# Optimization experiments

Measured on AMD Instinct MI355X. Metric: run time of the kernel, lower is better.

## Reference

```python
import jax, jax.numpy as jnp
import numpy as np

B, N, DIM, H, DH, M = 2, 2048, 1024, 16, 64, 512
INNER = H * DH  # 1024
KV = M + 1 + N  # xl mem + null kv + sequence = 2561


def rotate_half(x):
    x1, x2 = jnp.split(x, 2, axis=-1)
    return jnp.concatenate([-x2, x1], axis=-1)


def apply_rotary_pos_emb(pos, t):
    return t * jnp.cos(pos) + rotate_half(t) * jnp.sin(pos)


def setup_inputs() -> dict:
    key = jax.random.key(0)
    ks = jax.random.split(key, 8)
    return {
        "x": jax.random.normal(ks[0], (B, N, DIM), jnp.float32),
        "rotary_q": jax.random.uniform(ks[1], (N, DH), jnp.float32) * 6.28,
        "rotary_k": jax.random.uniform(ks[2], (KV, DH), jnp.float32) * 6.28,
        "xl_memories": jax.random.normal(ks[3], (2, B, H, M, DH), jnp.float32) * 0.02,
        "Wq": jax.random.normal(ks[4], (DIM, INNER), jnp.float32) * 0.02,
        "Wkv": jax.random.normal(ks[5], (DIM, 2 * INNER), jnp.float32) * 0.02,
        "Wout": jax.random.normal(ks[6], (INNER, INNER), jnp.float32) * 0.02,
        "null_kv": jax.random.normal(ks[7], (2, H, DH), jnp.float32),
    }


def reference(x, rotary_q, rotary_k, xl_memories, Wq, Wkv, Wout, null_kv):
    # QKV projections (no bias, matching keras Dense(use_bias=False))
    q = (x @ Wq).reshape(B, N, H, DH).transpose(0, 2, 1, 3)  # b h n d
    k, v = jnp.split(x @ Wkv, 2, axis=-1)
    k = k.reshape(B, N, H, DH).transpose(0, 2, 1, 3)
    v = v.reshape(B, N, H, DH).transpose(0, 2, 1, 3)

    # prepend learned null key/value (1 token)
    nk = jnp.broadcast_to(null_kv[0][None, :, None, :], (B, H, 1, DH))
    nv = jnp.broadcast_to(null_kv[1][None, :, None, :], (B, H, 1, DH))
    k = jnp.concatenate([nk, k], axis=2)
    v = jnp.concatenate([nv, v], axis=2)

    next_xl_memories = jnp.stack([k, v])  # [2, b, h, 1+n, d]

    # prepend XL memories along key axis
    k = jnp.concatenate([xl_memories[0], k], axis=2)  # b h kv d
    v = jnp.concatenate([xl_memories[1], v], axis=2)

    # inline rotary embedding on q and (full) k
    q = apply_rotary_pos_emb(rotary_q, q)
    k = apply_rotary_pos_emb(rotary_k, k)

    # causal attention with bottom-right aligned mask (mem/null tokens visible)
    scale = DH ** -0.5
    sim = jnp.einsum('bhid,bhjd->bhij', q, k) * scale  # b h n kv
    i = jnp.arange(N)[:, None]
    j = jnp.arange(KV)[None, :]
    causal_ok = j <= (i + (KV - N))
    sim = jnp.where(causal_ok, sim, jnp.finfo(sim.dtype).min)
    attn = jax.nn.softmax(sim, axis=-1)
    out = jnp.einsum('bhij,bhjd->bhid', attn, v)  # b h n d

    out = out.transpose(0, 2, 1, 3).reshape(B, N, INNER)
    return out @ Wout, next_xl_memories
```

## Files before the change

kernel.cpp:

```cpp
#include <hip/hip_runtime.h>
#include <hip/hip_bf16.h>


typedef short v8s __attribute__((ext_vector_type(8)));
typedef float v4f __attribute__((ext_vector_type(4)));

__device__ __forceinline__ float bf2f(unsigned short x) {
  return __uint_as_float(((unsigned)x) << 16);
}
__device__ __forceinline__ unsigned short f2bf(float f) {
  unsigned u = __float_as_uint(f);
  u += 0x7FFFu + ((u >> 16) & 1u);
  return (unsigned short)(u >> 16);
}

#if __has_builtin(__builtin_amdgcn_exp2f)
#define EXP2(x) __builtin_amdgcn_exp2f(x)
#else
#define EXP2(x) exp2f(x)
#endif

__device__ __forceinline__ void gld_lds16(const void* g, void* l) {
  __builtin_amdgcn_global_load_lds(
      (const __attribute__((address_space(1))) unsigned int*)g,
      (__attribute__((address_space(3))) unsigned int*)l, 16, 0, 0);
}

__device__ __forceinline__ unsigned pk_bf16(float lo, float hi) {
  union { __hip_bfloat162 h; unsigned u; } cv;
  cv.h = __float22bfloat162_rn(make_float2(lo, hi));
  return cv.u;
}

__global__ __launch_bounds__(256) void cvt_bf16(
    const float* __restrict__ S, unsigned short* __restrict__ D, int n4)
{
  const int i = blockIdx.x * 256 + threadIdx.x;
  if (i < n4) {
    const float4 v = ((const float4*)S)[i];
    ushort4 o;
    o.x = f2bf(v.x); o.y = f2bf(v.y); o.z = f2bf(v.z); o.w = f2bf(v.w);
    ((ushort4*)D)[i] = o;
  }
}

template <typename CT>
__global__ __launch_bounds__(256, 2) void gemm_bf16(
    const unsigned short* __restrict__ A,
    const unsigned short* __restrict__ WT,
    CT* __restrict__ C,
    int K, int ldc)
{
  __shared__ unsigned short As[128 * 64];
  __shared__ unsigned short Bs[128 * 64];
  const int tid  = threadIdx.x;
  const int wave = tid >> 6, lane = tid & 63;
  const int l15  = lane & 15, quad = lane >> 4;
  const int wm   = wave >> 1, wn = wave & 1;
  const int row0 = blockIdx.x * 128, col0 = blockIdx.y * 128;
  const int lrow = lane >> 3;
  const int gsw  = (lane & 7) ^ lrow;

  v4f acc[4][4];
  const v4f vzero = {0.f, 0.f, 0.f, 0.f};
#pragma unroll
  for (int i = 0; i < 4; ++i)
#pragma unroll
    for (int j = 0; j < 4; ++j) acc[i][j] = vzero;

  for (int k0 = 0; k0 < K; k0 += 64) {
    __syncthreads();
#pragma unroll
    for (int ro = 0; ro < 4; ++ro) {
      const int chunk = wave * 4 + ro;
      const int arow  = chunk * 8 + lrow;
      gld_lds16(A  + (size_t)(row0 + arow) * K + k0 + gsw * 8, As + chunk * 512);
      gld_lds16(WT + (size_t)(col0 + arow) * K + k0 + gsw * 8, Bs + chunk * 512);
    }
    __syncthreads();

    v8s af[4][2], bf[4][2];
#pragma unroll
    for (int tm = 0; tm < 4; ++tm) {
      const int r = wm * 64 + tm * 16 + l15;
#pragma unroll
      for (int kk = 0; kk < 2; ++kk) {
        const int slot = (kk * 4 + quad) ^ (r & 7);
        af[tm][kk] = *(const v8s*)(As + r * 64 + slot * 8);
      }
    }
#pragma unroll
    for (int tn = 0; tn < 4; ++tn) {
      const int r = wn * 64 + tn * 16 + l15;
#pragma unroll
      for (int kk = 0; kk < 2; ++kk) {
        const int slot = (kk * 4 + quad) ^ (r & 7);
        bf[tn][kk] = *(const v8s*)(Bs + r * 64 + slot * 8);
      }
    }
#pragma unroll
    for (int kk = 0; kk < 2; ++kk)
#pragma unroll
      for (int tm = 0; tm < 4; ++tm)
#pragma unroll
        for (int tn = 0; tn < 4; ++tn)
          acc[tm][tn] = __builtin_amdgcn_mfma_f32_16x16x32_bf16(
              af[tm][kk], bf[tn][kk], acc[tm][tn], 0, 0, 0);
  }

#pragma unroll
  for (int tm = 0; tm < 4; ++tm)
#pragma unroll
    for (int tn = 0; tn < 4; ++tn)
#pragma unroll
      for (int r = 0; r < 4; ++r) {
        const int row = row0 + wm * 64 + tm * 16 + quad * 4 + r;
        const int col = col0 + wn * 64 + tn * 16 + l15;
        if constexpr (sizeof(CT) == 2)
          C[(size_t)row * ldc + col] = (CT)f2bf(acc[tm][tn][r]);
        else
          C[(size_t)row * ldc + col] = (CT)acc[tm][tn][r];
      }
}

__global__ __launch_bounds__(256) void transpose_wt(
    const float* __restrict__ S0,
    const float* __restrict__ S1,
    int c0, int c1, int K,
    unsigned short* __restrict__ D)
{
  __shared__ float T[64][65];
  const int k0 = blockIdx.x * 64, n0 = blockIdx.y * 64;
  const int tid = threadIdx.x;
#pragma unroll
  for (int ro = 0; ro < 4; ++ro) {
    const int idx = ro * 256 + tid;
    const int kr = idx >> 4, ch = idx & 15;
    const int n = n0 + ch * 4;
    float4 val;
    if (n < c0) val = *(const float4*)(S0 + (size_t)(k0 + kr) * c0 + n);
    else        val = *(const float4*)(S1 + (size_t)(k0 + kr) * c1 + (n - c0));
    T[kr][ch * 4 + 0] = val.x; T[kr][ch * 4 + 1] = val.y;
    T[kr][ch * 4 + 2] = val.z; T[kr][ch * 4 + 3] = val.w;
  }
  __syncthreads();
#pragma unroll
  for (int ro = 0; ro < 2; ++ro) {
    const int idx = ro * 256 + tid;
    const int nl = idx >> 3, ch = idx & 7;
    __align__(16) unsigned short tmp[8];
#pragma unroll
    for (int e = 0; e < 8; ++e) tmp[e] = f2bf(T[ch * 8 + e][nl]);
    *(uint4*)(D + (size_t)(n0 + nl) * K + k0 + ch * 8) = *(const uint4*)tmp;
  }
}

__global__ __launch_bounds__(256) void assemble(
    const unsigned short* __restrict__ QKV,
    const float* __restrict__ rq,
    const float* __restrict__ rk,
    const float* __restrict__ xlm,
    const float* __restrict__ nkv,
    unsigned short* __restrict__ Qrot,
    unsigned short* __restrict__ Kf,
    unsigned short* __restrict__ Vn,
    float* __restrict__ nxl)
{
  const int gw = blockIdx.x * 4 + (threadIdx.x >> 6);
  const int d  = threadIdx.x & 63;
  const int RK = 32 * 2561;
  const int RQ = 32 * 2048;
  if (gw < RK) {
    const int bh = gw / 2561;
    const int j  = gw - bh * 2561;
    const int b  = bh >> 4, h = bh & 15;
    float kx, vx;
    if (j < 512) {
      const size_t i0 = (((size_t)(b * 16 + h)) * 512 + j) * 64 + d;
      kx = xlm[i0];
      vx = xlm[1048576 + i0];
    } else if (j == 512) {
      kx = nkv[h * 64 + d];
      vx = nkv[1024 + h * 64 + d];
    } else {
      const size_t rowb = ((size_t)(b * 2048 + (j - 513))) * 3072;
      kx = bf2f(QKV[rowb + 1024 + h * 64 + d]);
      vx = bf2f(QKV[rowb + 2048 + h * 64 + d]);
    }
    Vn[(((size_t)bh) * 2561 + j) * 64 + d] = f2bf(vx);
    if (j >= 512) {
      const size_t o0 = (((size_t)(b * 16 + h)) * 2049 + (j - 512)) * 64 + d;
      nxl[o0] = kx;
      nxl[4196352 + o0] = vx;
    }
    const float ang = rk[j * 64 + d];
    const float cs = __cosf(ang), sn = __sinf(ang);
    const float part = __shfl_xor(kx, 32);
    const float kr = kx * cs + (d < 32 ? -part : part) * sn;
    Kf[(((size_t)bh) * 2624 + j) * 64 + d] = f2bf(kr);
  } else if (gw < RK + RQ) {
    const int g2 = gw - RK;
    const int bh = g2 >> 11, n = g2 & 2047;
    const int b  = bh >> 4, h = bh & 15;
    const float qx = bf2f(QKV[((size_t)(b * 2048 + n)) * 3072 + h * 64 + d]);
    const float ang = rq[n * 64 + d];
    const float cs = __cosf(ang), sn = __sinf(ang);
    const float part = __shfl_xor(qx, 32);
    const float qr = qx * cs + (d < 32 ? -part : part) * sn;
    Qrot[(((size_t)bh) * 2048 + n) * 64 + d] = f2bf(qr * 0.18033688f);
  } else {
    const int g3 = gw - RK - RQ;
    const int bh = g3 / 63;
    const int jj = 2561 + (g3 - bh * 63);
    Kf[(((size_t)bh) * 2624 + jj) * 64 + d] = 0;
  }
}

__global__ __launch_bounds__(256) void transpose_v(
    const unsigned short* __restrict__ Vn,
    unsigned short* __restrict__ VTp)
{
  __shared__ unsigned short T[64][72];
  const int j0 = blockIdx.x * 64;
  const int bh = blockIdx.y;
  const int tid = threadIdx.x;
#pragma unroll
  for (int ro = 0; ro < 2; ++ro) {
    const int idx = ro * 256 + tid;
    const int jr = idx >> 3, ch = idx & 7;
    uint4 val = make_uint4(0, 0, 0, 0);
    if (j0 + jr < 2561)
      val = *(const uint4*)(Vn + (((size_t)bh) * 2561 + j0 + jr) * 64 + ch * 8);
    *(uint4*)(&T[jr][ch * 8]) = val;
  }
  __syncthreads();
#pragma unroll
  for (int ro = 0; ro < 2; ++ro) {
    const int idx = ro * 256 + tid;
    const int dl = idx >> 3, ch = idx & 7;
    __align__(16) unsigned short tmp[8];
#pragma unroll
    for (int e = 0; e < 8; ++e) {
      const int kappa = ch * 8 + e;
      const int sig = (kappa & 32) + ((e & 4) << 2) + ((ch & 3) << 2) + (e & 3);
      tmp[e] = T[sig][dl];
    }
    *(uint4*)(VTp + (((size_t)bh) * 64 + dl) * 2624 + j0 + ch * 8) = *(const uint4*)tmp;
  }
}

__global__ __launch_bounds__(256, 4) void attn_fa(
    const unsigned short* __restrict__ Qr,
    const unsigned short* __restrict__ Kf,
    const unsigned short* __restrict__ VTp,
    unsigned short* __restrict__ Ao)
{
  const int bh = blockIdx.y;
  const int qb = 31 - (int)((blockIdx.x + blockIdx.y) & 31);
  const int b = bh >> 4, h = bh & 15;
  __shared__ unsigned short Ks[2][2][32 * 72];
  __shared__ unsigned short Vs[2][2][64 * 40];
  const int tid = threadIdx.x;
  const int wave = tid >> 6;
  const int wr  = wave & 1;
  const int kvh = wave >> 1;
  const int lane = tid & 63;
  const int l15 = lane & 15, quad = lane >> 4;
  const v4f vzero = {0.f, 0.f, 0.f, 0.f};

  v8s qf00, qf01, qf10, qf11;
  {
    const unsigned short* Qg0 =
        Qr + (((size_t)bh) * 2048 + qb * 64 + wr * 32 + l15) * 64;
    qf00 = *(const v8s*)(Qg0 + quad * 8);
    qf01 = *(const v8s*)(Qg0 + 32 + quad * 8);
    const unsigned short* Qg1 = Qg0 + 16 * 64;
    qf10 = *(const v8s*)(Qg1 + quad * 8);
    qf11 = *(const v8s*)(Qg1 + 32 + quad * 8);
  }
  const int qb0 = qb * 64 + wr * 32 + l15 + 513;

  v4f O00 = vzero, O01 = vzero, O02 = vzero, O03 = vzero;
  v4f O10 = vzero, O11 = vzero, O12 = vzero, O13 = vzero;
  v4f Ol0 = vzero, Ol1 = vzero;
  const short one_bf = (short)0x3F80;
  const v8s ones = {one_bf, one_bf, one_bf, one_bf,
                    one_bf, one_bf, one_bf, one_bf};

  const unsigned short* Kg0 = Kf + (size_t)bh * 2624 * 64;
  const unsigned short* Vg0 = VTp + (size_t)bh * 64 * 2624;
  const int nt32  = (2 * qb + 19 <= 81) ? (2 * qb + 19) : 81;
  const int nh    = (nt32 + 1) >> 1;
  const int tbase = kvh ? nh : 0;
  const int tcnt  = kvh ? (nt32 - nh) : nh;
  const int tfast = 2 * qb + wr + 15;

  const int ptid = tid & 127;
  const int krow = ptid >> 3, ksch = ptid & 7;
  const int vrow = ptid >> 2, vscv = ptid & 3;
  uint4 kk0, kk1, vv0, vv1;

#define PREFETCH(t)                                                          \
  {                                                                          \
    const int j0p = (t) * 32;                                                \
    kk0 = *(const uint4*)(Kg0 + (size_t)(j0p + krow)      * 64 + ksch * 8);  \
    kk1 = *(const uint4*)(Kg0 + (size_t)(j0p + krow + 16) * 64 + ksch * 8);  \
    vv0 = *(const uint4*)(Vg0 + (size_t)(vrow)      * 2624 + j0p + vscv * 8);\
    vv1 = *(const uint4*)(Vg0 + (size_t)(vrow + 32) * 2624 + j0p + vscv * 8);\
  }
#define STAGE(bi)                                                            \
  {                                                                          \
    *(uint4*)(Ks[kvh][bi] + (krow)      * 72 + ksch * 8) = kk0;              \
    *(uint4*)(Ks[kvh][bi] + (krow + 16) * 72 + ksch * 8) = kk1;              \
    *(uint4*)(Vs[kvh][bi] + (vrow)      * 40 + vscv * 8) = vv0;              \
    *(uint4*)(Vs[kvh][bi] + (vrow + 32) * 40 + vscv * 8) = vv1;              \
  }

  auto compute_tile = [&](const unsigned short* Ksb, const unsigned short* Vsb,
                          int t) {
    v4f s00, s01, s10, s11;
    {
      const v8s ka0 = *(const v8s*)(Ksb + l15 * 72 + quad * 8);
      const v8s ka1 = *(const v8s*)(Ksb + l15 * 72 + 32 + quad * 8);
      v4f c = vzero;
      c = __builtin_amdgcn_mfma_f32_16x16x32_bf16(ka0, qf00, c, 0, 0, 0);
      c = __builtin_amdgcn_mfma_f32_16x16x32_bf16(ka1, qf01, c, 0, 0, 0);
      s00 = c;
      c = vzero;
      c = __builtin_amdgcn_mfma_f32_16x16x32_bf16(ka0, qf10, c, 0, 0, 0);
      c = __builtin_amdgcn_mfma_f32_16x16x32_bf16(ka1, qf11, c, 0, 0, 0);
      s10 = c;
      const v8s kb0 = *(const v8s*)(Ksb + (16 + l15) * 72 + quad * 8);
      const v8s kb1 = *(const v8s*)(Ksb + (16 + l15) * 72 + 32 + quad * 8);
      c = vzero;
      c = __builtin_amdgcn_mfma_f32_16x16x32_bf16(kb0, qf00, c, 0, 0, 0);
      c = __builtin_amdgcn_mfma_f32_16x16x32_bf16(kb1, qf01, c, 0, 0, 0);
      s01 = c;
      c = vzero;
      c = __builtin_amdgcn_mfma_f32_16x16x32_bf16(kb0, qf10, c, 0, 0, 0);
      c = __builtin_amdgcn_mfma_f32_16x16x32_bf16(kb1, qf11, c, 0, 0, 0);
      s11 = c;
    }

    if (t > tfast) {
      const int j0 = t * 32 + quad * 4;
#pragma unroll
      for (int r = 0; r < 4; ++r) {
        s00[r] = (j0 + r      <= qb0)      ? s00[r] : -1e30f;
        s01[r] = (j0 + 16 + r <= qb0)      ? s01[r] : -1e30f;
        s10[r] = (j0 + r      <= qb0 + 16) ? s10[r] : -1e30f;
        s11[r] = (j0 + 16 + r <= qb0 + 16) ? s11[r] : -1e30f;
      }
    }

    union PK { unsigned u[4]; v8s s8; };
    PK p0, p1;
    p0.u[0] = pk_bf16(EXP2(s00[0]), EXP2(s00[1]));
    p0.u[1] = pk_bf16(EXP2(s00[2]), EXP2(s00[3]));
    p0.u[2] = pk_bf16(EXP2(s01[0]), EXP2(s01[1]));
    p0.u[3] = pk_bf16(EXP2(s01[2]), EXP2(s01[3]));
    p1.u[0] = pk_bf16(EXP2(s10[0]), EXP2(s10[1]));
    p1.u[1] = pk_bf16(EXP2(s10[2]), EXP2(s10[3]));
    p1.u[2] = pk_bf16(EXP2(s11[0]), EXP2(s11[1]));
    p1.u[3] = pk_bf16(EXP2(s11[2]), EXP2(s11[3]));

    {
      const v8s vf0 = *(const v8s*)(Vsb + l15 * 40 + quad * 8);
      O00 = __builtin_amdgcn_mfma_f32_16x16x32_bf16(p0.s8, vf0, O00, 0, 0, 0);
      O10 = __builtin_amdgcn_mfma_f32_16x16x32_bf16(p1.s8, vf0, O10, 0, 0, 0);
      const v8s vf1 = *(const v8s*)(Vsb + (16 + l15) * 40 + quad * 8);
      O01 = __builtin_amdgcn_mfma_f32_16x16x32_bf16(p0.s8, vf1, O01, 0, 0, 0);
      O11 = __builtin_amdgcn_mfma_f32_16x16x32_bf16(p1.s8, vf1, O11, 0, 0, 0);
      const v8s vf2 = *(const v8s*)(Vsb + (32 + l15) * 40 + quad * 8);
      O02 = __builtin_amdgcn_mfma_f32_16x16x32_bf16(p0.s8, vf2, O02, 0, 0, 0);
      O12 = __builtin_amdgcn_mfma_f32_16x16x32_bf16(p1.s8, vf2, O12, 0, 0, 0);
      const v8s vf3 = *(const v8s*)(Vsb + (48 + l15) * 40 + quad * 8);
      O03 = __builtin_amdgcn_mfma_f32_16x16x32_bf16(p0.s8, vf3, O03, 0, 0, 0);
      O13 = __builtin_amdgcn_mfma_f32_16x16x32_bf16(p1.s8, vf3, O13, 0, 0, 0);
    }
    Ol0 = __builtin_amdgcn_mfma_f32_16x16x32_bf16(p0.s8, ones, Ol0, 0, 0, 0);
    Ol1 = __builtin_amdgcn_mfma_f32_16x16x32_bf16(p1.s8, ones, Ol1, 0, 0, 0);
  };

  PREFETCH(tbase);
  STAGE(0);
  PREFETCH(tbase + 1);
  __syncthreads();
  for (int it = 0; it < nh; ++it) {
    if (it < tcnt) {
      if (it + 1 < tcnt) {
        STAGE((it + 1) & 1);
        if (it + 2 < tcnt) PREFETCH(tbase + it + 2);
      }
      compute_tile(Ks[kvh][it & 1], Vs[kvh][it & 1], tbase + it);
    }
    __syncthreads();
  }
#undef PREFETCH
#undef STAGE

  float* R = (float*)(&Vs[0][0][0]);
  float* Rb = R + ((size_t)wr * 64 + lane) * 40;
  if (kvh == 1) {
    *(v4f*)(Rb + 0)  = O00; *(v4f*)(Rb + 4)  = O01;
    *(v4f*)(Rb + 8)  = O02; *(v4f*)(Rb + 12) = O03;
    *(v4f*)(Rb + 16) = O10; *(v4f*)(Rb + 20) = O11;
    *(v4f*)(Rb + 24) = O12; *(v4f*)(Rb + 28) = O13;
    *(v4f*)(Rb + 32) = Ol0; *(v4f*)(Rb + 36) = Ol1;
  }
  __syncthreads();
  if (kvh == 0) {
    O00 += *(const v4f*)(Rb + 0);  O01 += *(const v4f*)(Rb + 4);
    O02 += *(const v4f*)(Rb + 8);  O03 += *(const v4f*)(Rb + 12);
    O10 += *(const v4f*)(Rb + 16); O11 += *(const v4f*)(Rb + 20);
    O12 += *(const v4f*)(Rb + 24); O13 += *(const v4f*)(Rb + 28);
    Ol0 += *(const v4f*)(Rb + 32); Ol1 += *(const v4f*)(Rb + 36);
#pragma unroll
    for (int r = 0; r < 4; ++r) {
      const float linv0 = 1.0f / Ol0[r];
      const int n0 = qb * 64 + wr * 32 + quad * 4 + r;
      const size_t rb0 = ((size_t)b * 2048 + n0) * 1024 + h * 64;
      Ao[rb0 + 0 * 16 + l15] = f2bf(O00[r] * linv0);
      Ao[rb0 + 1 * 16 + l15] = f2bf(O01[r] * linv0);
      Ao[rb0 + 2 * 16 + l15] = f2bf(O02[r] * linv0);
      Ao[rb0 + 3 * 16 + l15] = f2bf(O03[r] * linv0);
      const float linv1 = 1.0f / Ol1[r];
      const size_t rb1 = rb0 + (size_t)16 * 1024;
      Ao[rb1 + 0 * 16 + l15] = f2bf(O10[r] * linv1);
      Ao[rb1 + 1 * 16 + l15] = f2bf(O11[r] * linv1);
      Ao[rb1 + 2 * 16 + l15] = f2bf(O12[r] * linv1);
      Ao[rb1 + 3 * 16 + l15] = f2bf(O13[r] * linv1);
    }
  }
}

extern "C" void kernel_launch(void* const* d_in, const int* in_sizes, int n_in,
                              void* d_out, int out_size, void* d_ws, size_t ws_size,
                              hipStream_t stream)
{
  const float* x    = (const float*)d_in[0];
  const float* rq   = (const float*)d_in[1];
  const float* rk   = (const float*)d_in[2];
  const float* xlm  = (const float*)d_in[3];
  const float* Wq   = (const float*)d_in[4];
  const float* Wkv  = (const float*)d_in[5];
  const float* Wout = (const float*)d_in[6];
  const float* nkv  = (const float*)d_in[7];
  float* out = (float*)d_out;
  float* nxl = out + 4194304;
  char* ws = (char*)d_ws;
  unsigned short* QKV   = (unsigned short*)(ws + 0);
  unsigned short* xbf   = (unsigned short*)(ws + 25165824);
  unsigned short* Ao    = (unsigned short*)(ws + 25165824);
  unsigned short* WqkvT = (unsigned short*)(ws + 33554432);
  unsigned short* WoutT = (unsigned short*)(ws + 39845888);
  unsigned short* Qrot  = (unsigned short*)(ws + 41943040);
  unsigned short* Kf    = (unsigned short*)(ws + 50331648);
  unsigned short* Vn    = (unsigned short*)(ws + 61079552);
  unsigned short* VTp   = (unsigned short*)(ws + 71569408);

  cvt_bf16<<<4096, 256, 0, stream>>>(x, xbf, 1048576);
  transpose_wt<<<dim3(16, 48), 256, 0, stream>>>(Wq, Wkv, 1024, 2048, 1024, WqkvT);
  transpose_wt<<<dim3(16, 16), 256, 0, stream>>>(Wout, Wout, 1024, 1024, 1024, WoutT);
  gemm_bf16<unsigned short><<<dim3(32, 24), 256, 0, stream>>>(xbf, WqkvT, QKV, 1024, 3072);
  assemble<<<37376, 256, 0, stream>>>(QKV, rq, rk, xlm, nkv, Qrot, Kf, Vn, nxl);
  transpose_v<<<dim3(41, 32), 256, 0, stream>>>(Vn, VTp);
  attn_fa<<<dim3(32, 32), 256, 0, stream>>>(Qrot, Kf, VTp, Ao);
  gemm_bf16<float><<<dim3(32, 8), 256, 0, stream>>>(Ao, WoutT, out, 1024, 1024);
}
```

Before: 243.0 us.

## Add 64-row output GEMM and hoist LDS loads with MFMA priority in attention

Adds a gemm_bf16_64 kernel with 64x128 tiles for the output projection, which doubles the block count (512 instead of 256) so the final 4096x1024 GEMM fills the CUs better. In the attention kernel, the K and V fragment LDS reads are moved ahead of their MFMA chains, and those chains are wrapped in s_setprio(1)/s_setprio(0) so the waves issuing matrix ops get scheduling priority. This trades higher register pressure from the hoisted loads, plus smaller per-block reuse in the GEMM, for better latency hiding and wave interleaving.

```diff
diff --git a/kernel.cpp b/kernel.cpp
--- a/kernel.cpp
+++ b/kernel.cpp
@@ -120,6 +120,86 @@
           C[(size_t)row * ldc + col] = (CT)f2bf(acc[tm][tn][r]);
         else
           C[(size_t)row * ldc + col] = (CT)acc[tm][tn][r];
+      }
+}
+
+__global__ __launch_bounds__(256, 2) void gemm_bf16_64(
+    const unsigned short* __restrict__ A,
+    const unsigned short* __restrict__ WT,
+    float* __restrict__ C,
+    int K, int ldc)
+{
+  __shared__ unsigned short As[64 * 64];
+  __shared__ unsigned short Bs[128 * 64];
+  const int tid  = threadIdx.x;
+  const int wave = tid >> 6, lane = tid & 63;
+  const int l15  = lane & 15, quad = lane >> 4;
+  const int wm   = wave >> 1, wn = wave & 1;
+  const int row0 = blockIdx.x * 64, col0 = blockIdx.y * 128;
+  const int lrow = lane >> 3;
+  const int gsw  = (lane & 7) ^ lrow;
+
+  v4f acc[2][4];
+  const v4f vzero = {0.f, 0.f, 0.f, 0.f};
+#pragma unroll
+  for (int i = 0; i < 2; ++i)
+#pragma unroll
+    for (int j = 0; j < 4; ++j) acc[i][j] = vzero;
+
+  for (int k0 = 0; k0 < K; k0 += 64) {
+    __syncthreads();
+#pragma unroll
+    for (int ro = 0; ro < 2; ++ro) {
+      const int chunk = wave * 2 + ro;
+      const int arow  = chunk * 8 + lrow;
+      gld_lds16(A + (size_t)(row0 + arow) * K + k0 + gsw * 8, As + chunk * 512);
+    }
+#pragma unroll
+    for (int ro = 0; ro < 4; ++ro) {
+      const int chunk = wave * 4 + ro;
+      const int brow  = chunk * 8 + lrow;
+      gld_lds16(WT + (size_t)(col0 + brow) * K + k0 + gsw * 8, Bs + chunk * 512);
+    }
+    __syncthreads();
+
+    v8s af[2][2], bf[4][2];
+#pragma unroll
+    for (int tm = 0; tm < 2; ++tm) {
+      const int r = wm * 32 + tm * 16 + l15;
+#pragma unroll
+      for (int kk = 0; kk < 2; ++kk) {
+        const int slot = (kk * 4 + quad) ^ (r & 7);
+        af[tm][kk] = *(const v8s*)(As + r * 64 + slot * 8);
+      }
+    }
+#pragma unroll
+    for (int tn = 0; tn < 4; ++tn) {
+      const int r = wn * 64 + tn * 16 + l15;
+#pragma unroll
+      for (int kk = 0; kk < 2; ++kk) {
+        const int slot = (kk * 4 + quad) ^ (r & 7);
+        bf[tn][kk] = *(const v8s*)(Bs + r * 64 + slot * 8);
+      }
+    }
+#pragma unroll
+    for (int kk = 0; kk < 2; ++kk)
+#pragma unroll
+      for (int tm = 0; tm < 2; ++tm)
+#pragma unroll
+        for (int tn = 0; tn < 4; ++tn)
+          acc[tm][tn] = __builtin_amdgcn_mfma_f32_16x16x32_bf16(
+              af[tm][kk], bf[tn][kk], acc[tm][tn], 0, 0, 0);
+  }
+
+#pragma unroll
+  for (int tm = 0; tm < 2; ++tm)
+#pragma unroll
+    for (int tn = 0; tn < 4; ++tn)
+#pragma unroll
+      for (int r = 0; r < 4; ++r) {
+        const int row = row0 + wm * 32 + tm * 16 + quad * 4 + r;
+        const int col = col0 + wn * 64 + tn * 16 + l15;
+        C[(size_t)row * ldc + col] = acc[tm][tn][r];
       }
 }
 
@@ -322,6 +402,9 @@
     {
       const v8s ka0 = *(const v8s*)(Ksb + l15 * 72 + quad * 8);
       const v8s ka1 = *(const v8s*)(Ksb + l15 * 72 + 32 + quad * 8);
+      const v8s kb0 = *(const v8s*)(Ksb + (16 + l15) * 72 + quad * 8);
+      const v8s kb1 = *(const v8s*)(Ksb + (16 + l15) * 72 + 32 + quad * 8);
+      __builtin_amdgcn_s_setprio(1);
       v4f c = vzero;
       c = __builtin_amdgcn_mfma_f32_16x16x32_bf16(ka0, qf00, c, 0, 0, 0);
       c = __builtin_amdgcn_mfma_f32_16x16x32_bf16(ka1, qf01, c, 0, 0, 0);
@@ -330,8 +413,6 @@
       c = __builtin_amdgcn_mfma_f32_16x16x32_bf16(ka0, qf10, c, 0, 0, 0);
       c = __builtin_amdgcn_mfma_f32_16x16x32_bf16(ka1, qf11, c, 0, 0, 0);
       s10 = c;
-      const v8s kb0 = *(const v8s*)(Ksb + (16 + l15) * 72 + quad * 8);
-      const v8s kb1 = *(const v8s*)(Ksb + (16 + l15) * 72 + 32 + quad * 8);
       c = vzero;
       c = __builtin_amdgcn_mfma_f32_16x16x32_bf16(kb0, qf00, c, 0, 0, 0);
       c = __builtin_amdgcn_mfma_f32_16x16x32_bf16(kb1, qf01, c, 0, 0, 0);
@@ -340,6 +421,7 @@
       c = __builtin_amdgcn_mfma_f32_16x16x32_bf16(kb0, qf10, c, 0, 0, 0);
       c = __builtin_amdgcn_mfma_f32_16x16x32_bf16(kb1, qf11, c, 0, 0, 0);
       s11 = c;
+      __builtin_amdgcn_s_setprio(0);
     }
 
     if (t > tfast) {
@@ -366,20 +448,22 @@
 
     {
       const v8s vf0 = *(const v8s*)(Vsb + l15 * 40 + quad * 8);
+      const v8s vf1 = *(const v8s*)(Vsb + (16 + l15) * 40 + quad * 8);
+      const v8s vf2 = *(const v8s*)(Vsb + (32 + l15) * 40 + quad * 8);
+      const v8s vf3 = *(const v8s*)(Vsb + (48 + l15) * 40 + quad * 8);
+      __builtin_amdgcn_s_setprio(1);
       O00 = __builtin_amdgcn_mfma_f32_16x16x32_bf16(p0.s8, vf0, O00, 0, 0, 0);
       O10 = __builtin_amdgcn_mfma_f32_16x16x32_bf16(p1.s8, vf0, O10, 0, 0, 0);
-      const v8s vf1 = *(const v8s*)(Vsb + (16 + l15) * 40 + quad * 8);
       O01 = __builtin_amdgcn_mfma_f32_16x16x32_bf16(p0.s8, vf1, O01, 0, 0, 0);
       O11 = __builtin_amdgcn_mfma_f32_16x16x32_bf16(p1.s8, vf1, O11, 0, 0, 0);
-      const v8s vf2 = *(const v8s*)(Vsb + (32 + l15) * 40 + quad * 8);
       O02 = __builtin_amdgcn_mfma_f32_16x16x32_bf16(p0.s8, vf2, O02, 0, 0, 0);
       O12 = __builtin_amdgcn_mfma_f32_16x16x32_bf16(p1.s8, vf2, O12, 0, 0, 0);
-      const v8s vf3 = *(const v8s*)(Vsb + (48 + l15) * 40 + quad * 8);
       O03 = __builtin_amdgcn_mfma_f32_16x16x32_bf16(p0.s8, vf3, O03, 0, 0, 0);
       O13 = __builtin_amdgcn_mfma_f32_16x16x32_bf16(p1.s8, vf3, O13, 0, 0, 0);
-    }
-    Ol0 = __builtin_amdgcn_mfma_f32_16x16x32_bf16(p0.s8, ones, Ol0, 0, 0, 0);
-    Ol1 = __builtin_amdgcn_mfma_f32_16x16x32_bf16(p1.s8, ones, Ol1, 0, 0, 0);
+      Ol0 = __builtin_amdgcn_mfma_f32_16x16x32_bf16(p0.s8, ones, Ol0, 0, 0, 0);
+      Ol1 = __builtin_amdgcn_mfma_f32_16x16x32_bf16(p1.s8, ones, Ol1, 0, 0, 0);
+      __builtin_amdgcn_s_setprio(0);
+    }
   };
 
   PREFETCH(tbase);
@@ -466,5 +550,5 @@
   assemble<<<37376, 256, 0, stream>>>(QKV, rq, rk, xlm, nkv, Qrot, Kf, Vn, nxl);
   transpose_v<<<dim3(41, 32), 256, 0, stream>>>(Vn, VTp);
   attn_fa<<<dim3(32, 32), 256, 0, stream>>>(Qrot, Kf, VTp, Ao);
-  gemm_bf16<float><<<dim3(32, 8), 256, 0, stream>>>(Ao, WoutT, out, 1024, 1024);
-}
+  gemm_bf16_64<<<dim3(64, 8), 256, 0, stream>>>(Ao, WoutT, out, 1024, 1024);
+}
```

After: 231.2 us. -4.9%, faster.
